# Kernel tuning notes

Hardware: AMD Instinct MI355X
Metric: run time of the kernel (lower is better)

Reference implementation:

```python
import jax, jax.numpy as jnp
from jax import lax
import numpy as np

WINDOW_SIZES = (1, 2, 3)


def _proj(x, w1, b1, w2, b2):
    # gated projection: sigmoid(Linear1) * tanh(Linear2)
    return jax.nn.sigmoid(x @ w1.T + b1) * jnp.tanh(x @ w2.T + b2)


def setup_inputs() -> dict:
    key = jax.random.key(0)
    ks = jax.random.split(key, 16)
    V, E, D = 50000, 1024, 1024
    N, La, Lq = 64, 512, 64
    s = 0.02  # weight scale to keep sigmoid/tanh unsaturated
    return {
        "data_q": jax.random.randint(ks[0], (Lq,), 0, V),
        "data_as": jax.random.randint(ks[1], (N, La), 0, V),
        "emb": jax.random.normal(ks[2], (V, E), jnp.float32),
        "w1": jax.random.normal(ks[3], (D, E), jnp.float32) * s,
        "b1": jnp.zeros((D,), jnp.float32),
        "w2": jax.random.normal(ks[4], (D, E), jnp.float32) * s,
        "b2": jnp.zeros((D,), jnp.float32),
        "cw1": jax.random.normal(ks[5], (D, D, 1), jnp.float32) * s,
        "cb1": jnp.zeros((D,), jnp.float32),
        "cw2": jax.random.normal(ks[6], (D, D, 2), jnp.float32) * s,
        "cb2": jnp.zeros((D,), jnp.float32),
        "cw3": jax.random.normal(ks[7], (D, D, 3), jnp.float32) * s,
        "cb3": jnp.zeros((D,), jnp.float32),
        "lin_w": jax.random.normal(ks[8], (D, 3 * D), jnp.float32) * s,
        "lin_b": jnp.zeros((D,), jnp.float32),
        "soft_w": jax.random.normal(ks[9], (1, D), jnp.float32) * s,
        "soft_b": jnp.zeros((1,), jnp.float32),
    }


def reference(data_q, data_as, emb, w1, b1, w2, b2,
              cw1, cb1, cw2, cb2, cw3, cb3, lin_w, lin_b, soft_w, soft_b):
    N, La = data_as.shape
    a_tok = data_as.reshape(-1)                     # [T] concatenated answers
    emb_a = emb[a_tok]                              # [T, E]
    emb_q = emb[data_q]                             # [Lq, E]
    pa = _proj(emb_a, w1, b1, w2, b2)               # [T, D]
    pq = _proj(emb_q, w1, b1, w2, b2)               # [Lq, D]

    # attention: M_r = q @ a^T ; alpha = softmax over question positions
    M = pq @ pa.T                                   # [Lq, T]
    alpha = jax.nn.softmax(M.T, axis=1)             # [T, Lq]
    Y = alpha @ pq                                  # [T, D]
    sim = pa * Y                                    # elementwise compare (mul)

    starts = jnp.arange(N) * La
    x = sim.T[None]                                 # [1, D, T]
    pools = []
    for w, cw, cb in zip(WINDOW_SIZES, (cw1, cw2, cw3), (cb1, cb2, cb3)):
        conv = lax.conv_general_dilated(
            x, cw, (1,), 'VALID',
            dimension_numbers=('NCW', 'OIW', 'NCW'))[0].T + cb  # [T-w+1, D]
        conv = jax.nn.relu(conv)
        # DMax: per-answer max over rows [start_k, start_k + La - w + 1)
        idx = starts[:, None] + jnp.arange(La - w + 1)[None, :]  # [N, La-w+1]
        pools.append(conv[idx].max(axis=1))          # [N, D]

    cat = jnp.concatenate(pools, axis=1)            # [N, 3D]
    h = jnp.tanh(cat @ lin_w.T + lin_b)             # [N, D]
    logits = (h @ soft_w.T + soft_b).reshape(-1)    # [N]
    return jax.nn.log_softmax(logits)
```

## Files before the change

### kernel.cpp

```cpp
#include <hip/hip_runtime.h>

#define DEV __device__ __forceinline__

typedef __bf16 bf16x8 __attribute__((ext_vector_type(8)));
typedef float f32x4 __attribute__((ext_vector_type(4)));
typedef unsigned short u16;
typedef u16 u16x4 __attribute__((ext_vector_type(4)));

constexpr int T_ANS = 32768;
constexpr int LQ    = 64;
constexpr int M_ALL = T_ANS + LQ;
constexpr int M_PAD = 33024;
constexpr int DIM   = 1024;

DEV u16 f2bf(float x) {
  unsigned u = __float_as_uint(x);
  return (u16)((u + 0x7FFFu + ((u >> 16) & 1u)) >> 16);
}
DEV float bf2f(u16 s) { return __uint_as_float(((unsigned)s) << 16); }

DEV void gl2lds16(const void* g, void* l) {
  __builtin_amdgcn_global_load_lds(
      (const __attribute__((address_space(1))) unsigned int*)g,
      (__attribute__((address_space(3))) unsigned int*)l, 16, 0, 0);
}

#define MF(A, B, C) __builtin_amdgcn_mfma_f32_16x16x32_bf16(A, B, C, 0, 0, 0)


DEV void stageC(const char* gk, char* ldsT, int row0, int tid) {
  const int f = tid << 4;
  const int r = row0 + (f >> 7);
  const int cb = ((f >> 4) & 7) ^ (r & 7);
  gl2lds16(gk + (size_t)r * 2048 + (cb << 4), ldsT + (row0 << 7) + f);
}

DEV bf16x8 LF(const char* ldsT, int row, int cbyte) {
  return *(const bf16x8*)(ldsT + (row << 7) + (cbyte ^ ((row & 7) << 4)));
}

#define MQUAD(Q, a00, a01, a10, a11)                                                  \
    acc[2*(Q)][0] = MF(a00, bb00, acc[2*(Q)][0]); acc[2*(Q)][0] = MF(a01, bb01, acc[2*(Q)][0]); \
    acc[2*(Q)][1] = MF(a00, bb10, acc[2*(Q)][1]); acc[2*(Q)][1] = MF(a01, bb11, acc[2*(Q)][1]); \
    acc[2*(Q)][2] = MF(a00, bb20, acc[2*(Q)][2]); acc[2*(Q)][2] = MF(a01, bb21, acc[2*(Q)][2]); \
    acc[2*(Q)][3] = MF(a00, bb30, acc[2*(Q)][3]); acc[2*(Q)][3] = MF(a01, bb31, acc[2*(Q)][3]); \
    acc[2*(Q)+1][0] = MF(a10, bb00, acc[2*(Q)+1][0]); acc[2*(Q)+1][0] = MF(a11, bb01, acc[2*(Q)+1][0]); \
    acc[2*(Q)+1][1] = MF(a10, bb10, acc[2*(Q)+1][1]); acc[2*(Q)+1][1] = MF(a11, bb11, acc[2*(Q)+1][1]); \
    acc[2*(Q)+1][2] = MF(a10, bb20, acc[2*(Q)+1][2]); acc[2*(Q)+1][2] = MF(a11, bb21, acc[2*(Q)+1][2]); \
    acc[2*(Q)+1][3] = MF(a10, bb30, acc[2*(Q)+1][3]); acc[2*(Q)+1][3] = MF(a11, bb31, acc[2*(Q)+1][3]);

#define PHB(LA, LB, STAGES, VMW)                                                      \
  {                                                                                   \
    bb00 = LF(LB, wn +  0 + lr, hi16); bb01 = LF(LB, wn +  0 + lr, 64 + hi16);        \
    bb10 = LF(LB, wn + 16 + lr, hi16); bb11 = LF(LB, wn + 16 + lr, 64 + hi16);        \
    bb20 = LF(LB, wn + 32 + lr, hi16); bb21 = LF(LB, wn + 32 + lr, 64 + hi16);        \
    bb30 = LF(LB, wn + 48 + lr, hi16); bb31 = LF(LB, wn + 48 + lr, 64 + hi16);        \
    bf16x8 a00 = LF(LA, wm + lr, hi16),      a01 = LF(LA, wm + lr, 64 + hi16);        \
    bf16x8 a10 = LF(LA, wm + 16 + lr, hi16), a11 = LF(LA, wm + 16 + lr, 64 + hi16);   \
    STAGES                                                                            \
    __builtin_amdgcn_s_barrier();                                                     \
    asm volatile("s_waitcnt lgkmcnt(0)" ::: "memory");                                \
    __builtin_amdgcn_sched_barrier(0);                                                \
    __builtin_amdgcn_s_setprio(1);                                                    \
    MQUAD(0, a00, a01, a10, a11)                                                      \
    __builtin_amdgcn_s_setprio(0);                                                    \
    VMW                                                                               \
    __builtin_amdgcn_s_barrier();                                                     \
  }

#define PHA(Q, LA, STAGES, VMW)                                                       \
  {                                                                                   \
    bf16x8 a00 = LF(LA, wm + (2*(Q))*16 + lr, hi16);                                  \
    bf16x8 a01 = LF(LA, wm + (2*(Q))*16 + lr, 64 + hi16);                             \
    bf16x8 a10 = LF(LA, wm + (2*(Q)+1)*16 + lr, hi16);                                \
    bf16x8 a11 = LF(LA, wm + (2*(Q)+1)*16 + lr, 64 + hi16);                           \
    STAGES                                                                            \
    __builtin_amdgcn_s_barrier();                                                     \
    asm volatile("s_waitcnt lgkmcnt(0)" ::: "memory");                                \
    __builtin_amdgcn_sched_barrier(0);                                                \
    __builtin_amdgcn_s_setprio(1);                                                    \
    MQUAD(Q, a00, a01, a10, a11)                                                      \
    __builtin_amdgcn_s_setprio(0);                                                    \
    VMW                                                                               \
    __builtin_amdgcn_s_barrier();                                                     \
  }

#define VM2 asm volatile("s_waitcnt vmcnt(2)" ::: "memory"); __builtin_amdgcn_sched_barrier(0);
#define VM0 asm volatile("s_waitcnt vmcnt(0)" ::: "memory"); __builtin_amdgcn_sched_barrier(0);

#define GROUP(LA, LB, S1, S2, S3, VMW)                                                \
  PHB(LA, LB, S1, )                                                                   \
  PHA(1, LA, S2, )                                                                    \
  PHA(2, LA, S3, )                                                                    \
  PHA(3, LA, , VMW)

#define GEMM_PIPE(KT)                                                                 \
  const char* A0 = lds;            const char* B0c = lds + 32768;                     \
  const char* A1 = lds + 65536;    const char* B1c = lds + 98304;                     \
  char* A0w = lds; char* B0w = lds + 32768; char* A1w = lds + 65536; char* B1w = lds + 98304; \
  f32x4 acc[8][4] = {};                                                               \
  bf16x8 bb00, bb01, bb10, bb11, bb20, bb21, bb30, bb31;                              \
  stageC(Ab(0), A0w, 0, tid);   stageC(Ab(0), A0w, 128, tid);                         \
  stageC(Ab(0), A0w, 64, tid);  stageC(Ab(0), A0w, 192, tid);                         \
  stageC(Bb(0), B0w, 0, tid);   stageC(Bb(0), B0w, 64, tid);                          \
  stageC(Bb(0), B0w, 128, tid); stageC(Bb(0), B0w, 192, tid);                         \
  stageC(Ab(1), A1w, 0, tid);   stageC(Ab(1), A1w, 128, tid);                         \
  VM2                                                                                 \
  __builtin_amdgcn_s_barrier();                                                       \
  for (int i = 0; i < (KT)/2 - 1; ++i) {                                              \
    const int kt1 = 2*i + 1;                                                          \
    GROUP(A0, B0c,                                                                    \
      stageC(Ab(kt1), A1w, 64, tid);  stageC(Ab(kt1), A1w, 192, tid);                 \
      stageC(Bb(kt1), B1w, 0, tid);   stageC(Bb(kt1), B1w, 64, tid); ,                \
      stageC(Bb(kt1), B1w, 128, tid); stageC(Bb(kt1), B1w, 192, tid); ,               \
      stageC(Ab(kt1+1), A0w, 0, tid); stageC(Ab(kt1+1), A0w, 128, tid); ,             \
      VM2)                                                                            \
    GROUP(A1, B1c,                                                                    \
      stageC(Ab(kt1+1), A0w, 64, tid); stageC(Ab(kt1+1), A0w, 192, tid);              \
      stageC(Bb(kt1+1), B0w, 0, tid);  stageC(Bb(kt1+1), B0w, 64, tid); ,             \
      stageC(Bb(kt1+1), B0w, 128, tid); stageC(Bb(kt1+1), B0w, 192, tid); ,           \
      stageC(Ab(kt1+2), A1w, 0, tid); stageC(Ab(kt1+2), A1w, 128, tid); ,             \
      VM2)                                                                            \
  }                                                                                   \
  {                                                                                   \
    const int kt1 = (KT) - 1;                                                         \
    GROUP(A0, B0c,                                                                    \
      stageC(Ab(kt1), A1w, 64, tid);  stageC(Ab(kt1), A1w, 192, tid);                 \
      stageC(Bb(kt1), B1w, 0, tid);   stageC(Bb(kt1), B1w, 64, tid); ,                \
      stageC(Bb(kt1), B1w, 128, tid); stageC(Bb(kt1), B1w, 192, tid); ,               \
      ,                                                                               \
      VM0)                                                                            \
    GROUP(A1, B1c, , , , )                                                            \
  }


__global__ void cast4(const float* __restrict__ src, u16* __restrict__ dst, int n4) {
  int i = blockIdx.x * 256 + threadIdx.x;
  if (i < n4) {
    float4 v = ((const float4*)src)[i];
    u16x4 o = { f2bf(v.x), f2bf(v.y), f2bf(v.z), f2bf(v.w) };
    ((u16x4*)dst)[i] = o;
  }
}

template<int W>
__global__ void cast_conv_w(const float* __restrict__ src, u16* __restrict__ dst) {
  int i = blockIdx.x * 256 + threadIdx.x;
  if (i < 1024 * 1024) {
#pragma unroll
    for (int k = 0; k < W; ++k)
      dst[(size_t)k * (1024 * 1024) + i] = f2bf(src[(size_t)i * W + k]);
  }
}

__global__ void pack_w12(const float* __restrict__ w1, const float* __restrict__ w2,
                         u16* __restrict__ W12) {
  int i = blockIdx.x * 256 + threadIdx.x;
  if (i < 2048 * 1024) {
    int n2 = i >> 10, k = i & 1023;
    int j = n2 >> 4, m = n2 & 15;
    const float* src = (j & 1) ? w2 : w1;
    W12[i] = f2bf(src[(size_t)((j >> 1) * 16 + m) * 1024 + k]);
  }
}

__global__ void gather_cast(const int* __restrict__ dq, const int* __restrict__ das,
                            const float* __restrict__ emb, u16* __restrict__ X) {
  const int row = blockIdx.x;
  const int c   = threadIdx.x;
  size_t dsto = (size_t)row * DIM + c * 4;
  if (row >= M_ALL) {
    u16x4 z = {0, 0, 0, 0};
    *(u16x4*)(X + dsto) = z;
    return;
  }
  const int tok = (row < T_ANS) ? das[row] : dq[row - T_ANS];
  float4 v = ((const float4*)(emb + (size_t)tok * DIM))[c];
  u16x4 o = { f2bf(v.x), f2bf(v.y), f2bf(v.z), f2bf(v.w) };
  *(u16x4*)(X + dsto) = o;
}

__global__ void transpose_pq(const u16* __restrict__ pa, u16* __restrict__ pqT) {
  int i = blockIdx.x * 256 + threadIdx.x;
  int e = i >> 6, q = i & 63;
  pqT[i] = pa[(size_t)(T_ANS + q) * DIM + e];
}

__global__ void zero_pad_sim(u16* __restrict__ sim) {
  int i = blockIdx.x * 256 + threadIdx.x;
  if (i < 2 * DIM) sim[(size_t)T_ANS * DIM + i] = 0;
}

__global__ void cast_cat(const float* __restrict__ cat, u16* __restrict__ catb) {
  int i = blockIdx.x * 256 + threadIdx.x;
  if (i < 128 * 3072) {
    int row = i / 3072;
    catb[i] = (row < 64) ? f2bf(cat[i]) : (u16)0;
  }
}


__global__ __launch_bounds__(512, 1)
void proj_g(const u16* __restrict__ X, const u16* __restrict__ W12,
            const float* __restrict__ b1, const float* __restrict__ b2,
            u16* __restrict__ pa) {
  extern __shared__ char lds[];
  const int tid = threadIdx.x, lane = tid & 63;
  const int wid = tid >> 6;
  const int wm = (wid >> 2) * 128, wn = (wid & 3) * 64;
  const int lr = lane & 15, hi16 = (lane >> 4) * 16;
  const int wg = ((int)blockIdx.x % 8) * 129 + (int)blockIdx.x / 8;
  const int tm = (wg >> 3) * 256, tn = (wg & 7) * 256;
  const char* Ag = (const char*)X + (size_t)tm * 2048;
  const char* Bg = (const char*)W12 + (size_t)tn * 2048;
  auto Ab = [&](int kt) { return Ag + (kt >> 4) * 2048 + ((kt & 15) << 7); };
  auto Bb = [&](int kt) { return Bg + (size_t)(kt >> 4) * 2097152 + ((kt & 15) << 7); };

  GEMM_PIPE(16)

  u16* cw = (u16*)lds;
  const int lg = (lane >> 4) * 4;
#pragma unroll
  for (int pp = 0; pp < 2; ++pp) {
    const int clocal = ((wn >> 5) + pp) * 16 + lr;
    const int col = (tn >> 1) + clocal;
    const float b1v = b1[col], b2v = b2[col];
#pragma unroll
    for (int mi = 0; mi < 8; ++mi)
#pragma unroll
      for (int r = 0; r < 4; ++r) {
        const int rowL = wm + mi * 16 + lg + r;
        const float x1 = acc[mi][2 * pp][r] + b1v;
        const float x2 = acc[mi][2 * pp + 1][r] + b2v;
        const float sg = 1.f / (1.f + __expf(-x1));
        const float th = 2.f / (1.f + __expf(-2.f * x2)) - 1.f;
        cw[rowL * 132 + clocal] = f2bf(sg * th);
      }
  }
  __syncthreads();
#pragma unroll
  for (int it = 0; it < 16; ++it) {
    const int cid = it * 512 + tid;
    const int rowL = cid >> 5, c4 = (cid & 31) * 4;
    u16x4 v = *(const u16x4*)(cw + rowL * 132 + c4);
    *(u16x4*)(pa + (size_t)(tm + rowL) * DIM + (tn >> 1) + c4) = v;
  }
}


template<int W>
__global__ __launch_bounds__(512, 1)
void conv_g(const u16* __restrict__ sim, const u16* __restrict__ Bw,
            const float* __restrict__ cb, float* __restrict__ cat) {
  extern __shared__ char lds[];
  const int tid = threadIdx.x, lane = tid & 63;
  const int wid = tid >> 6;
  const int wm = (wid >> 2) * 128, wn = (wid & 3) * 64;
  const int lr = lane & 15, hi16 = (lane >> 4) * 16;
  const int wg = ((int)blockIdx.x % 8) * 64 + (int)blockIdx.x / 8;
  const int tm = (wg >> 2) * 256, tn = (wg & 3) * 256;
  const char* Ag = (const char*)sim + (size_t)tm * 2048;
  const char* Bg = (const char*)Bw + (size_t)tn * 2048;
  auto Ab = [&](int kt) { return Ag + (kt >> 4) * 2048 + ((kt & 15) << 7); };
  auto Bb = [&](int kt) { return Bg + (size_t)(kt >> 4) * 2097152 + ((kt & 15) << 7); };

  GEMM_PIPE(16 * W)

  const int lg = (lane >> 4) * 4;
  const int n = tm >> 9;
#pragma unroll
  for (int ni = 0; ni < 4; ++ni) {
    const int col = tn + wn + ni * 16 + lr;
    const float cbv = cb[col];
    float vmax = 0.f;
#pragma unroll
    for (int mi = 0; mi < 8; ++mi)
#pragma unroll
      for (int r = 0; r < 4; ++r) {
        const int t = tm + wm + mi * 16 + lg + r;
        float v = fmaxf(acc[mi][ni][r] + cbv, 0.f);
        if ((t & 511) > 512 - W) v = 0.f;
        vmax = fmaxf(vmax, v);
      }
    vmax = fmaxf(vmax, __shfl_xor(vmax, 16));
    vmax = fmaxf(vmax, __shfl_xor(vmax, 32));
    if (lane < 16)
      atomicMax((int*)&cat[(size_t)n * 3072 + (W - 1) * 1024 + col], __float_as_int(vmax));
  }
}


__global__ __launch_bounds__(256, 2)
void attn_s(const u16* __restrict__ pa, float* __restrict__ Spart) {
  __shared__ alignas(16) u16 sA[128 * 32];
  __shared__ alignas(16) u16 sB[64 * 32];
  const int tid = threadIdx.x, lane = tid & 63;
  const int tm = blockIdx.x * 128;
  const int kbase = blockIdx.y * 256;
  const int wid = tid >> 6;
  const int wm = (wid >> 1) * 64, wn = (wid & 1) * 32;
  const u16* pq = pa + (size_t)T_ANS * DIM;
  f32x4 acc[4][2] = {};
  for (int k0 = kbase; k0 < kbase + 256; k0 += 32) {
#pragma unroll
    for (int j = 0; j < 2; ++j) {
      const int f = tid * 16 + j * 4096;
      const int r = f >> 6, cb = f & 63;
      gl2lds16((const char*)pa + (size_t)(tm + r) * 2048 + k0 * 2 + cb, (char*)sA + f);
    }
    {
      const int f = tid * 16;
      const int r = f >> 6, cb = f & 63;
      gl2lds16((const char*)pq + (size_t)r * 2048 + k0 * 2 + cb, (char*)sB + f);
    }
    __syncthreads();
    const int lr = lane & 15, lk = (lane >> 4) * 8;
    bf16x8 af[4], bfr[2];
#pragma unroll
    for (int i = 0; i < 4; ++i)
      af[i] = *(const bf16x8*)(sA + (wm + i * 16 + lr) * 32 + lk);
#pragma unroll
    for (int i = 0; i < 2; ++i)
      bfr[i] = *(const bf16x8*)(sB + (wn + i * 16 + lr) * 32 + lk);
#pragma unroll
    for (int mi = 0; mi < 4; ++mi)
#pragma unroll
      for (int ni = 0; ni < 2; ++ni)
        acc[mi][ni] = MF(af[mi], bfr[ni], acc[mi][ni]);
    __syncthreads();
  }
  const int lr = lane & 15, lg = (lane >> 4) * 4;
  float* Sp = Spart + (size_t)blockIdx.y * (T_ANS * 64);
#pragma unroll
  for (int mi = 0; mi < 4; ++mi)
#pragma unroll
    for (int ni = 0; ni < 2; ++ni)
#pragma unroll
      for (int r = 0; r < 4; ++r) {
        const int row = tm + wm + mi * 16 + lg + r;
        const int col = wn + ni * 16 + lr;
        Sp[(size_t)row * 64 + col] = acc[mi][ni][r];
      }
}

__global__ void softmax64(const float* __restrict__ Spart, u16* __restrict__ alpha) {
  const int row = blockIdx.x * 4 + (threadIdx.x >> 6);
  const int lane = threadIdx.x & 63;
  const size_t o = (size_t)row * 64 + lane;
  float v = Spart[o] + Spart[(size_t)1 * T_ANS * 64 + o]
          + Spart[(size_t)2 * T_ANS * 64 + o] + Spart[(size_t)3 * T_ANS * 64 + o];
  float m = v;
#pragma unroll
  for (int o2 = 32; o2 > 0; o2 >>= 1) m = fmaxf(m, __shfl_xor(m, o2));
  const float e = __expf(v - m);
  float s = e;
#pragma unroll
  for (int o2 = 32; o2 > 0; o2 >>= 1) s += __shfl_xor(s, o2);
  alpha[(size_t)row * 64 + lane] = f2bf(e / s);
}


__global__ __launch_bounds__(256, 2)
void attn_y_sim(const u16* __restrict__ alpha, const u16* __restrict__ pqT,
                const u16* __restrict__ pa, u16* __restrict__ sim) {
  __shared__ alignas(16) u16 sA[128 * 32];
  __shared__ alignas(16) u16 sB[128 * 32];
  const int tid = threadIdx.x, lane = tid & 63;
  const int tm = blockIdx.x * 128, tn = blockIdx.y * 128;
  const int wid = tid >> 6;
  const int wm = (wid >> 1) * 64, wn = (wid & 1) * 64;
  f32x4 acc[4][4] = {};
  for (int k0 = 0; k0 < 64; k0 += 32) {
#pragma unroll
    for (int j = 0; j < 2; ++j) {
      const int f = tid * 16 + j * 4096;
      const int r = f >> 6, cb = f & 63;
      gl2lds16((const char*)alpha + (size_t)(tm + r) * 128 + k0 * 2 + cb, (char*)sA + f);
      gl2lds16((const char*)pqT   + (size_t)(tn + r) * 128 + k0 * 2 + cb, (char*)sB + f);
    }
    __syncthreads();
    const int lr = lane & 15, lk = (lane >> 4) * 8;
    bf16x8 af[4], bfr[4];
#pragma unroll
    for (int i = 0; i < 4; ++i) {
      af[i]  = *(const bf16x8*)(sA + (wm + i * 16 + lr) * 32 + lk);
      bfr[i] = *(const bf16x8*)(sB + (wn + i * 16 + lr) * 32 + lk);
    }
#pragma unroll
    for (int mi = 0; mi < 4; ++mi)
#pragma unroll
      for (int ni = 0; ni < 4; ++ni)
        acc[mi][ni] = MF(af[mi], bfr[ni], acc[mi][ni]);
    __syncthreads();
  }
  const int lr = lane & 15, lg = (lane >> 4) * 4;
#pragma unroll
  for (int ni = 0; ni < 4; ++ni) {
    const int col = tn + wn + ni * 16 + lr;
#pragma unroll
    for (int mi = 0; mi < 4; ++mi)
#pragma unroll
      for (int r = 0; r < 4; ++r) {
        const int row = tm + wm + mi * 16 + lg + r;
        const size_t o = (size_t)row * DIM + col;
        sim[o] = f2bf(bf2f(pa[o]) * acc[mi][ni][r]);
      }
  }
}


__global__ __launch_bounds__(256, 2)
void final_h(const u16* __restrict__ catb, const u16* __restrict__ linb,
             const float* __restrict__ lin_b, float* __restrict__ h) {
  __shared__ alignas(16) u16 sA[128 * 32];
  __shared__ alignas(16) u16 sB[128 * 32];
  const int tid = threadIdx.x, lane = tid & 63;
  const int tn = blockIdx.y * 128;
  const int wid = tid >> 6;
  const int wm = (wid >> 1) * 64, wn = (wid & 1) * 64;
  f32x4 acc[4][4] = {};
  for (int k0 = 0; k0 < 3072; k0 += 32) {
#pragma unroll
    for (int j = 0; j < 2; ++j) {
      const int f = tid * 16 + j * 4096;
      const int r = f >> 6, cb = f & 63;
      gl2lds16((const char*)catb + (size_t)r * 6144 + k0 * 2 + cb, (char*)sA + f);
      gl2lds16((const char*)linb + (size_t)(tn + r) * 6144 + k0 * 2 + cb, (char*)sB + f);
    }
    __syncthreads();
    const int lr = lane & 15, lk = (lane >> 4) * 8;
    bf16x8 af[4], bfr[4];
#pragma unroll
    for (int i = 0; i < 4; ++i) {
      af[i]  = *(const bf16x8*)(sA + (wm + i * 16 + lr) * 32 + lk);
      bfr[i] = *(const bf16x8*)(sB + (wn + i * 16 + lr) * 32 + lk);
    }
#pragma unroll
    for (int mi = 0; mi < 4; ++mi)
#pragma unroll
      for (int ni = 0; ni < 4; ++ni)
        acc[mi][ni] = MF(af[mi], bfr[ni], acc[mi][ni]);
    __syncthreads();
  }
  const int lr = lane & 15, lg = (lane >> 4) * 4;
#pragma unroll
  for (int ni = 0; ni < 4; ++ni) {
    const int col = tn + wn + ni * 16 + lr;
    const float bv = lin_b[col];
#pragma unroll
    for (int mi = 0; mi < 4; ++mi)
#pragma unroll
      for (int r = 0; r < 4; ++r) {
        const int row = wm + mi * 16 + lg + r;
        if (row < 64) {
          const float x = acc[mi][ni][r] + bv;
          h[(size_t)row * DIM + col] = 2.f / (1.f + __expf(-2.f * x)) - 1.f;
        }
      }
  }
}

__global__ void final_logits(const float* __restrict__ h, const float* __restrict__ soft_w,
                             const float* __restrict__ soft_b, float* __restrict__ out) {
  __shared__ float part[256];
  const int t = threadIdx.x;
  const int n = t >> 2, q = t & 3;
  float s = 0.f;
  for (int j = q * 256; j < q * 256 + 256; ++j) s += h[(size_t)n * DIM + j] * soft_w[j];
  part[t] = s;
  __syncthreads();
  if (t < 64) {
    float logit = part[t * 4] + part[t * 4 + 1] + part[t * 4 + 2] + part[t * 4 + 3] + soft_b[0];
    float m = logit;
#pragma unroll
    for (int o = 32; o > 0; o >>= 1) m = fmaxf(m, __shfl_xor(m, o));
    float e = __expf(logit - m);
    float ssum = e;
#pragma unroll
    for (int o = 32; o > 0; o >>= 1) ssum += __shfl_xor(ssum, o);
    out[t] = (logit - m) - logf(ssum);
  }
}


extern "C" void kernel_launch(void* const* d_in, const int* in_sizes, int n_in,
                              void* d_out, int out_size, void* d_ws, size_t ws_size,
                              hipStream_t stream) {
  const int*   data_q  = (const int*)d_in[0];
  const int*   data_as = (const int*)d_in[1];
  const float* emb     = (const float*)d_in[2];
  const float* w1      = (const float*)d_in[3];
  const float* b1      = (const float*)d_in[4];
  const float* w2      = (const float*)d_in[5];
  const float* b2      = (const float*)d_in[6];
  const float* cw1     = (const float*)d_in[7];
  const float* cb1     = (const float*)d_in[8];
  const float* cw2     = (const float*)d_in[9];
  const float* cb2     = (const float*)d_in[10];
  const float* cw3     = (const float*)d_in[11];
  const float* cb3     = (const float*)d_in[12];
  const float* lin_w   = (const float*)d_in[13];
  const float* lin_b   = (const float*)d_in[14];
  const float* soft_w  = (const float*)d_in[15];
  const float* soft_b  = (const float*)d_in[16];
  float* out = (float*)d_out;

  hipFuncSetAttribute((const void*)proj_g, hipFuncAttributeMaxDynamicSharedMemorySize, 131072);
  hipFuncSetAttribute((const void*)conv_g<1>, hipFuncAttributeMaxDynamicSharedMemorySize, 131072);
  hipFuncSetAttribute((const void*)conv_g<2>, hipFuncAttributeMaxDynamicSharedMemorySize, 131072);
  hipFuncSetAttribute((const void*)conv_g<3>, hipFuncAttributeMaxDynamicSharedMemorySize, 131072);

  u16* X     = (u16*)d_ws;
  u16* pa    = X    + (size_t)M_PAD * DIM;
  u16* W12   = pa   + (size_t)M_PAD * DIM;
  u16* cwb   = W12  + (size_t)2 * 1024 * 1024;
  u16* linb  = cwb  + (size_t)6 * 1024 * 1024;
  u16* pqT   = linb + (size_t)3 * 1024 * 1024;
  u16* alpha = pqT  + 64 * 1024;
  float* cat = (float*)(alpha + (size_t)T_ANS * 64);
  u16* catb  = (u16*)(cat + 64 * 3072);
  float* h   = (float*)(catb + 128 * 3072);
  u16* simb  = X;
  float* Spart = (float*)X;

  hipMemsetAsync(cat, 0, 64 * 3072 * sizeof(float), stream);

  pack_w12<<<8192, 256, 0, stream>>>(w1, w2, W12);
  cast4<<<3072, 256, 0, stream>>>(lin_w, linb, 3072 * 1024 / 4);
  cast_conv_w<1><<<4096, 256, 0, stream>>>(cw1, cwb);
  cast_conv_w<2><<<4096, 256, 0, stream>>>(cw2, cwb + (size_t)1 * 1024 * 1024);
  cast_conv_w<3><<<4096, 256, 0, stream>>>(cw3, cwb + (size_t)3 * 1024 * 1024);

  gather_cast<<<M_PAD, 256, 0, stream>>>(data_q, data_as, emb, X);

  proj_g<<<1032, 512, 131072, stream>>>(X, W12, b1, b2, pa);
  transpose_pq<<<256, 256, 0, stream>>>(pa, pqT);

  attn_s<<<dim3(T_ANS / 128, 4), 256, 0, stream>>>(pa, Spart);
  softmax64<<<T_ANS / 4, 256, 0, stream>>>(Spart, alpha);
  attn_y_sim<<<dim3(T_ANS / 128, 8), 256, 0, stream>>>(alpha, pqT, pa, simb);
  zero_pad_sim<<<8, 256, 0, stream>>>(simb);

  conv_g<1><<<512, 512, 131072, stream>>>(simb, cwb, cb1, cat);
  conv_g<2><<<512, 512, 131072, stream>>>(simb, cwb + (size_t)1 * 1024 * 1024, cb2, cat);
  conv_g<3><<<512, 512, 131072, stream>>>(simb, cwb + (size_t)3 * 1024 * 1024, cb3, cat);

  cast_cat<<<1536, 256, 0, stream>>>(cat, catb);
  final_h<<<dim3(1, 8), 256, 0, stream>>>(catb, linb, lin_b, h);
  final_logits<<<1, 256, 0, stream>>>(h, soft_w, soft_b, out);
}
```

Baseline: 786.2 us.

## Simplify GEMM pipeline to one-tile-ahead double buffering with reordered MFMAs

Replaces the unrolled two-group GEMM pipeline, which staggered staging across buffers and waited with vmcnt(2), with a plain loop over K tiles. Each iteration prefetches the whole next A and B tile into the alternate buffer during phases 0 and 1, then waits with vmcnt(0) at the end of the tile. It also reorders the MFMA chain so the two K-halves interleave across independent accumulators, adds an earlier partial lgkmcnt wait before the barrier, and drops the unused outer-K terms from the address lambdas. The aim is shorter MFMA dependency chains and simpler scheduling, at the cost of less overlap between global loads and compute.

```diff
diff --git a/kernel.cpp b/kernel.cpp
--- a/kernel.cpp
+++ b/kernel.cpp
@@ -40,14 +40,22 @@
 }
 
 #define MQUAD(Q, a00, a01, a10, a11)                                                  \
-    acc[2*(Q)][0] = MF(a00, bb00, acc[2*(Q)][0]); acc[2*(Q)][0] = MF(a01, bb01, acc[2*(Q)][0]); \
-    acc[2*(Q)][1] = MF(a00, bb10, acc[2*(Q)][1]); acc[2*(Q)][1] = MF(a01, bb11, acc[2*(Q)][1]); \
-    acc[2*(Q)][2] = MF(a00, bb20, acc[2*(Q)][2]); acc[2*(Q)][2] = MF(a01, bb21, acc[2*(Q)][2]); \
-    acc[2*(Q)][3] = MF(a00, bb30, acc[2*(Q)][3]); acc[2*(Q)][3] = MF(a01, bb31, acc[2*(Q)][3]); \
-    acc[2*(Q)+1][0] = MF(a10, bb00, acc[2*(Q)+1][0]); acc[2*(Q)+1][0] = MF(a11, bb01, acc[2*(Q)+1][0]); \
-    acc[2*(Q)+1][1] = MF(a10, bb10, acc[2*(Q)+1][1]); acc[2*(Q)+1][1] = MF(a11, bb11, acc[2*(Q)+1][1]); \
-    acc[2*(Q)+1][2] = MF(a10, bb20, acc[2*(Q)+1][2]); acc[2*(Q)+1][2] = MF(a11, bb21, acc[2*(Q)+1][2]); \
-    acc[2*(Q)+1][3] = MF(a10, bb30, acc[2*(Q)+1][3]); acc[2*(Q)+1][3] = MF(a11, bb31, acc[2*(Q)+1][3]);
+    acc[2*(Q)][0]   = MF(a00, bb00, acc[2*(Q)][0]);                                   \
+    acc[2*(Q)][1]   = MF(a00, bb10, acc[2*(Q)][1]);                                   \
+    acc[2*(Q)][2]   = MF(a00, bb20, acc[2*(Q)][2]);                                   \
+    acc[2*(Q)][3]   = MF(a00, bb30, acc[2*(Q)][3]);                                   \
+    acc[2*(Q)+1][0] = MF(a10, bb00, acc[2*(Q)+1][0]);                                 \
+    acc[2*(Q)+1][1] = MF(a10, bb10, acc[2*(Q)+1][1]);                                 \
+    acc[2*(Q)+1][2] = MF(a10, bb20, acc[2*(Q)+1][2]);                                 \
+    acc[2*(Q)+1][3] = MF(a10, bb30, acc[2*(Q)+1][3]);                                 \
+    acc[2*(Q)][0]   = MF(a01, bb01, acc[2*(Q)][0]);                                   \
+    acc[2*(Q)][1]   = MF(a01, bb11, acc[2*(Q)][1]);                                   \
+    acc[2*(Q)][2]   = MF(a01, bb21, acc[2*(Q)][2]);                                   \
+    acc[2*(Q)][3]   = MF(a01, bb31, acc[2*(Q)][3]);                                   \
+    acc[2*(Q)+1][0] = MF(a11, bb01, acc[2*(Q)+1][0]);                                 \
+    acc[2*(Q)+1][1] = MF(a11, bb11, acc[2*(Q)+1][1]);                                 \
+    acc[2*(Q)+1][2] = MF(a11, bb21, acc[2*(Q)+1][2]);                                 \
+    acc[2*(Q)+1][3] = MF(a11, bb31, acc[2*(Q)+1][3]);
 
 #define PHB(LA, LB, STAGES, VMW)                                                      \
   {                                                                                   \
@@ -58,6 +66,7 @@
     bf16x8 a00 = LF(LA, wm + lr, hi16),      a01 = LF(LA, wm + lr, 64 + hi16);        \
     bf16x8 a10 = LF(LA, wm + 16 + lr, hi16), a11 = LF(LA, wm + 16 + lr, 64 + hi16);   \
     STAGES                                                                            \
+    asm volatile("s_waitcnt lgkmcnt(8)" ::: "memory");                                \
     __builtin_amdgcn_s_barrier();                                                     \
     asm volatile("s_waitcnt lgkmcnt(0)" ::: "memory");                                \
     __builtin_amdgcn_sched_barrier(0);                                                \
@@ -85,52 +94,38 @@
     __builtin_amdgcn_s_barrier();                                                     \
   }
 
-#define VM2 asm volatile("s_waitcnt vmcnt(2)" ::: "memory"); __builtin_amdgcn_sched_barrier(0);
 #define VM0 asm volatile("s_waitcnt vmcnt(0)" ::: "memory"); __builtin_amdgcn_sched_barrier(0);
 
-#define GROUP(LA, LB, S1, S2, S3, VMW)                                                \
-  PHB(LA, LB, S1, )                                                                   \
-  PHA(1, LA, S2, )                                                                    \
-  PHA(2, LA, S3, )                                                                    \
-  PHA(3, LA, , VMW)
-
 #define GEMM_PIPE(KT)                                                                 \
-  const char* A0 = lds;            const char* B0c = lds + 32768;                     \
-  const char* A1 = lds + 65536;    const char* B1c = lds + 98304;                     \
-  char* A0w = lds; char* B0w = lds + 32768; char* A1w = lds + 65536; char* B1w = lds + 98304; \
   f32x4 acc[8][4] = {};                                                               \
   bf16x8 bb00, bb01, bb10, bb11, bb20, bb21, bb30, bb31;                              \
-  stageC(Ab(0), A0w, 0, tid);   stageC(Ab(0), A0w, 128, tid);                         \
-  stageC(Ab(0), A0w, 64, tid);  stageC(Ab(0), A0w, 192, tid);                         \
-  stageC(Bb(0), B0w, 0, tid);   stageC(Bb(0), B0w, 64, tid);                          \
-  stageC(Bb(0), B0w, 128, tid); stageC(Bb(0), B0w, 192, tid);                         \
-  stageC(Ab(1), A1w, 0, tid);   stageC(Ab(1), A1w, 128, tid);                         \
-  VM2                                                                                 \
+  stageC(Ab(0), lds, 0, tid);           stageC(Ab(0), lds, 64, tid);                  \
+  stageC(Ab(0), lds, 128, tid);         stageC(Ab(0), lds, 192, tid);                 \
+  stageC(Bb(0), lds + 32768, 0, tid);   stageC(Bb(0), lds + 32768, 64, tid);          \
+  stageC(Bb(0), lds + 32768, 128, tid); stageC(Bb(0), lds + 32768, 192, tid);         \
+  VM0                                                                                 \
   __builtin_amdgcn_s_barrier();                                                       \
-  for (int i = 0; i < (KT)/2 - 1; ++i) {                                              \
-    const int kt1 = 2*i + 1;                                                          \
-    GROUP(A0, B0c,                                                                    \
-      stageC(Ab(kt1), A1w, 64, tid);  stageC(Ab(kt1), A1w, 192, tid);                 \
-      stageC(Bb(kt1), B1w, 0, tid);   stageC(Bb(kt1), B1w, 64, tid); ,                \
-      stageC(Bb(kt1), B1w, 128, tid); stageC(Bb(kt1), B1w, 192, tid); ,               \
-      stageC(Ab(kt1+1), A0w, 0, tid); stageC(Ab(kt1+1), A0w, 128, tid); ,             \
-      VM2)                                                                            \
-    GROUP(A1, B1c,                                                                    \
-      stageC(Ab(kt1+1), A0w, 64, tid); stageC(Ab(kt1+1), A0w, 192, tid);              \
-      stageC(Bb(kt1+1), B0w, 0, tid);  stageC(Bb(kt1+1), B0w, 64, tid); ,             \
-      stageC(Bb(kt1+1), B0w, 128, tid); stageC(Bb(kt1+1), B0w, 192, tid); ,           \
-      stageC(Ab(kt1+2), A1w, 0, tid); stageC(Ab(kt1+2), A1w, 128, tid); ,             \
-      VM2)                                                                            \
+  for (int kt = 0; kt < (KT) - 1; ++kt) {                                             \
+    const char* LA = (kt & 1) ? lds + 65536 : lds;                                    \
+    const char* LB = (kt & 1) ? lds + 98304 : lds + 32768;                            \
+    char* WA = (kt & 1) ? lds : lds + 65536;                                          \
+    char* WB = (kt & 1) ? lds + 32768 : lds + 98304;                                  \
+    PHB(LA, LB,                                                                       \
+        stageC(Ab(kt + 1), WA, 0, tid);   stageC(Ab(kt + 1), WA, 64, tid);            \
+        stageC(Ab(kt + 1), WA, 128, tid); stageC(Ab(kt + 1), WA, 192, tid); , )       \
+    PHA(1, LA,                                                                        \
+        stageC(Bb(kt + 1), WB, 0, tid);   stageC(Bb(kt + 1), WB, 64, tid);            \
+        stageC(Bb(kt + 1), WB, 128, tid); stageC(Bb(kt + 1), WB, 192, tid); , )       \
+    PHA(2, LA, , )                                                                    \
+    PHA(3, LA, , VM0)                                                                 \
   }                                                                                   \
   {                                                                                   \
-    const int kt1 = (KT) - 1;                                                         \
-    GROUP(A0, B0c,                                                                    \
-      stageC(Ab(kt1), A1w, 64, tid);  stageC(Ab(kt1), A1w, 192, tid);                 \
-      stageC(Bb(kt1), B1w, 0, tid);   stageC(Bb(kt1), B1w, 64, tid); ,                \
-      stageC(Bb(kt1), B1w, 128, tid); stageC(Bb(kt1), B1w, 192, tid); ,               \
-      ,                                                                               \
-      VM0)                                                                            \
-    GROUP(A1, B1c, , , , )                                                            \
+    const char* LA = (((KT) - 1) & 1) ? lds + 65536 : lds;                            \
+    const char* LB = (((KT) - 1) & 1) ? lds + 98304 : lds + 32768;                    \
+    PHB(LA, LB, , )                                                                   \
+    PHA(1, LA, , )                                                                    \
+    PHA(2, LA, , )                                                                    \
+    PHA(3, LA, , )                                                                    \
   }
 
 
@@ -213,8 +208,8 @@
   const int tm = (wg >> 3) * 256, tn = (wg & 7) * 256;
   const char* Ag = (const char*)X + (size_t)tm * 2048;
   const char* Bg = (const char*)W12 + (size_t)tn * 2048;
-  auto Ab = [&](int kt) { return Ag + (kt >> 4) * 2048 + ((kt & 15) << 7); };
-  auto Bb = [&](int kt) { return Bg + (size_t)(kt >> 4) * 2097152 + ((kt & 15) << 7); };
+  auto Ab = [&](int kt) { return Ag + ((kt & 15) << 7); };
+  auto Bb = [&](int kt) { return Bg + ((kt & 15) << 7); };
 
   GEMM_PIPE(16)
 
```

After: 772.7 us. No clear change (-1.7%).
